# Kernel tuning notes

Measured on AMD Instinct MI355X. Metric: run time of the kernel, lower is better.

The kernel has to match this reference:

```python
import jax, jax.numpy as jnp
import numpy as np

MAX_ITER = 10
EPS = 1e-4


def setup_inputs() -> dict:
    key = jax.random.key(0)
    k1, k2, k3 = jax.random.split(key, 3)
    B, N, M = 64, 1024, 1024
    s = jax.random.uniform(k1, (B, N, M), dtype=jnp.float32)
    nrows = jax.random.randint(k2, (B,), 0, N, dtype=jnp.int64 if jax.config.read('jax_enable_x64') else jnp.int32)
    ncols = jax.random.randint(k3, (B,), 0, M, dtype=nrows.dtype)
    return {"s": s, "nrows": nrows, "ncols": ncols}


def _sinkhorn(s, nrows, ncols):
    # Faithful to torch Sinkhorn.forward with exp=False, dummy_row=False.
    # The torch code builds [B,N,N]/[B,M,M] block-of-ones matrices and matmuls;
    # mathematically this is a masked column-sum (even iters) / row-sum (odd iters)
    # over the valid nrows[b] x ncols[b] block, followed by division inside the
    # block and zeroing outside it.
    B, N, M = s.shape
    row_mask = jnp.arange(N)[None, :] < nrows[:, None]            # [B, N]
    col_mask = jnp.arange(M)[None, :] < ncols[:, None]            # [B, M]
    mask = row_mask[:, :, None] & col_mask[:, None, :]            # [B, N, M]

    out = s + EPS
    for i in range(MAX_ITER):
        if i % 2 == 0:
            # column sums over valid rows -> [B, 1, M]
            sm = jnp.sum(jnp.where(row_mask[:, :, None], out, 0.0), axis=1, keepdims=True)
        else:
            # row sums over valid cols -> [B, N, 1]
            sm = jnp.sum(jnp.where(col_mask[:, None, :], out, 0.0), axis=2, keepdims=True)
        sm = jnp.where(sm == 0, 1.0, sm)  # guard (only affects masked-out entries)
        out = jnp.where(mask, out / sm, 0.0)
    return out


def reference(s, nrows, ncols):
    return _sinkhorn(s, nrows, ncols)
```

## Files before the change

### kernel.cpp

```cpp
#include <hip/hip_runtime.h>
#include <hip/hip_fp16.h>

#define EPS 1e-4f
constexpr int N_DIM = 1024;
constexpr int M_DIM = 1024;
constexpr int BATCH = 64;
constexpr int CH    = 16;
constexpr int CROWS = N_DIM / CH;


__global__ __launch_bounds__(256)
void conv_col0(const float* __restrict__ s,
               const int* __restrict__ nrows,
               const int* __restrict__ ncols,
               __half* __restrict__ h,
               float* __restrict__ tp0) {
    const int b  = blockIdx.y;
    const int mt = blockIdx.x & 3;
    const int ch = blockIdx.x >> 2;
    const int R = nrows[b], C = ncols[b];
    const int n0 = ch * CROWS;
    if (n0 >= R) return;
    const int lane = threadIdx.x & 63, wv = threadIdx.x >> 6;
    const int m = mt * 256 + lane * 4;
    const int nend = min(R, n0 + CROWS);
    const size_t base = (size_t)b * N_DIM * M_DIM;

    float4 acc = make_float4(0.f, 0.f, 0.f, 0.f);
    if (mt * 256 < C) {
        for (int n = n0 + wv; n < nend; n += 4) {
            float4 v = *(const float4*)(s + base + (size_t)n * M_DIM + m);
            v.x = (m + 0 < C) ? v.x + EPS : 0.f;
            v.y = (m + 1 < C) ? v.y + EPS : 0.f;
            v.z = (m + 2 < C) ? v.z + EPS : 0.f;
            v.w = (m + 3 < C) ? v.w + EPS : 0.f;
            acc.x += v.x; acc.y += v.y; acc.z += v.z; acc.w += v.w;
            union { __half2 h2[2]; uint2 u2; } pk;
            pk.h2[0] = __floats2half2_rn(v.x, v.y);
            pk.h2[1] = __floats2half2_rn(v.z, v.w);
            *(uint2*)(h + base + (size_t)n * M_DIM + m) = pk.u2;
        }
    } else {
        const uint2 z = make_uint2(0u, 0u);
        for (int n = n0 + wv; n < nend; n += 4)
            *(uint2*)(h + base + (size_t)n * M_DIM + m) = z;
    }
    __shared__ float4 red[4][64];
    red[wv][lane] = acc;
    __syncthreads();
    if (wv == 0) {
        float4 a0 = red[0][lane], a1 = red[1][lane],
               a2 = red[2][lane], a3 = red[3][lane];
        float4 t = make_float4(a0.x + a1.x + a2.x + a3.x,
                               a0.y + a1.y + a2.y + a3.y,
                               a0.z + a1.z + a2.z + a3.z,
                               a0.w + a1.w + a2.w + a3.w);
        *(float4*)(tp0 + (size_t)(ch * BATCH + b) * M_DIM + m) = t;
    }
}

template <bool FINAL>
__global__ __launch_bounds__(256)
void row_step(const __half* __restrict__ h,
              const int* __restrict__ nrows,
              const int* __restrict__ ncols,
              const float* __restrict__ tpIn,
              float* __restrict__ tpOut,
              float* __restrict__ out) {
    const int b  = blockIdx.y;
    const int ch = blockIdx.x;
    const int R = nrows[b], C = ncols[b];
    const int n0 = ch * CROWS;
    if (!FINAL && n0 >= R) return;
    const int lane = threadIdx.x & 63, wv = threadIdx.x >> 6;
    const size_t base = (size_t)b * N_DIM * M_DIM;
    const bool hi = (C > 512);
    const bool anyrows = (n0 < R);

    __shared__ float clds[M_DIM];
    __shared__ float tp_lds[4][M_DIM];

    float crlo[8], crhi[8];
    if (anyrows) {
        const int nch = min(CH, (R + CROWS - 1) / CROWS);
        const int t4 = threadIdx.x * 4;
        if (hi || t4 < 512) {
            float4 sum = make_float4(0.f, 0.f, 0.f, 0.f);
            for (int cc = 0; cc < nch; ++cc) {
                float4 p = *(const float4*)(tpIn + (size_t)(cc * BATCH + b) * M_DIM + t4);
                sum.x += p.x; sum.y += p.y; sum.z += p.z; sum.w += p.w;
            }
            float4 cv;
            cv.x = (sum.x == 0.f) ? 1.f : 1.f / sum.x;
            cv.y = (sum.y == 0.f) ? 1.f : 1.f / sum.y;
            cv.z = (sum.z == 0.f) ? 1.f : 1.f / sum.z;
            cv.w = (sum.w == 0.f) ? 1.f : 1.f / sum.w;
            *(float4*)&clds[t4] = cv;
        }
        __syncthreads();
        {
            float4 a = *(const float4*)&clds[lane * 8];
            float4 bb = *(const float4*)&clds[lane * 8 + 4];
            crlo[0]=a.x; crlo[1]=a.y; crlo[2]=a.z; crlo[3]=a.w;
            crlo[4]=bb.x; crlo[5]=bb.y; crlo[6]=bb.z; crlo[7]=bb.w;
            if (hi) {
                float4 d = *(const float4*)&clds[512 + lane * 8];
                float4 e = *(const float4*)&clds[512 + lane * 8 + 4];
                crhi[0]=d.x; crhi[1]=d.y; crhi[2]=d.z; crhi[3]=d.w;
                crhi[4]=e.x; crhi[5]=e.y; crhi[6]=e.z; crhi[7]=e.w;
            }
        }
    }

    float tplo[8] = {0,0,0,0,0,0,0,0};
    float tphi[8] = {0,0,0,0,0,0,0,0};

    for (int i = 0; i < 16; ++i) {
        const int n = n0 + wv * 16 + i;
        if (n < R) {
            const __half* hrow = h + base + (size_t)n * M_DIM;
            uint4 rlo = *(const uint4*)(hrow + lane * 8);
            float flo[8];
            {
                const __half2* hp = (const __half2*)&rlo;
#pragma unroll
                for (int k = 0; k < 4; ++k) {
                    float2 f = __half22float2(hp[k]);
                    flo[2*k] = f.x; flo[2*k+1] = f.y;
                }
            }
            float dot = 0.f;
#pragma unroll
            for (int k = 0; k < 8; ++k) dot += flo[k] * crlo[k];
            float fhi[8];
            if (hi) {
                uint4 rhi = *(const uint4*)(hrow + 512 + lane * 8);
                const __half2* hq = (const __half2*)&rhi;
#pragma unroll
                for (int k = 0; k < 4; ++k) {
                    float2 f = __half22float2(hq[k]);
                    fhi[2*k] = f.x; fhi[2*k+1] = f.y;
                }
#pragma unroll
                for (int k = 0; k < 8; ++k) dot += fhi[k] * crhi[k];
            }
#pragma unroll
            for (int off = 32; off; off >>= 1) dot += __shfl_xor(dot, off);
            const float r = (dot == 0.f) ? 1.f : 1.f / dot;

            if (FINAL) {
                float* orow = out + base + (size_t)n * M_DIM;
                float4 o0 = make_float4(flo[0]*r*crlo[0], flo[1]*r*crlo[1],
                                        flo[2]*r*crlo[2], flo[3]*r*crlo[3]);
                float4 o1 = make_float4(flo[4]*r*crlo[4], flo[5]*r*crlo[5],
                                        flo[6]*r*crlo[6], flo[7]*r*crlo[7]);
                *(float4*)(orow + lane * 8)     = o0;
                *(float4*)(orow + lane * 8 + 4) = o1;
                float4 o2 = make_float4(0.f,0.f,0.f,0.f), o3 = o2;
                if (hi) {
                    o2 = make_float4(fhi[0]*r*crhi[0], fhi[1]*r*crhi[1],
                                     fhi[2]*r*crhi[2], fhi[3]*r*crhi[3]);
                    o3 = make_float4(fhi[4]*r*crhi[4], fhi[5]*r*crhi[5],
                                     fhi[6]*r*crhi[6], fhi[7]*r*crhi[7]);
                }
                *(float4*)(orow + 512 + lane * 8)     = o2;
                *(float4*)(orow + 512 + lane * 8 + 4) = o3;
            } else {
#pragma unroll
                for (int k = 0; k < 8; ++k) tplo[k] += flo[k] * r;
                if (hi) {
#pragma unroll
                    for (int k = 0; k < 8; ++k) tphi[k] += fhi[k] * r;
                }
            }
        } else if (FINAL) {
            float* orow = out + base + (size_t)n * M_DIM;
            const float4 z = make_float4(0.f, 0.f, 0.f, 0.f);
            *(float4*)(orow + lane * 8)           = z;
            *(float4*)(orow + lane * 8 + 4)       = z;
            *(float4*)(orow + 512 + lane * 8)     = z;
            *(float4*)(orow + 512 + lane * 8 + 4) = z;
        }
    }

    if (!FINAL) {
#pragma unroll
        for (int k = 0; k < 8; ++k) tp_lds[wv][lane * 8 + k] = tplo[k];
        if (hi) {
#pragma unroll
            for (int k = 0; k < 8; ++k) tp_lds[wv][512 + lane * 8 + k] = tphi[k];
        }
        __syncthreads();
        const int t4 = threadIdx.x * 4;
        if (hi || t4 < 512) {
            float4 s0 = *(const float4*)&tp_lds[0][t4];
            float4 s1 = *(const float4*)&tp_lds[1][t4];
            float4 s2 = *(const float4*)&tp_lds[2][t4];
            float4 s3 = *(const float4*)&tp_lds[3][t4];
            float4 t = make_float4(s0.x+s1.x+s2.x+s3.x, s0.y+s1.y+s2.y+s3.y,
                                   s0.z+s1.z+s2.z+s3.z, s0.w+s1.w+s2.w+s3.w);
            *(float4*)(tpOut + (size_t)(ch * BATCH + b) * M_DIM + t4) = t;
        }
    }
}

template <bool FIRST, int CHUNKS>
__global__ __launch_bounds__(256)
void col_sweep(const float* __restrict__ s, const int* __restrict__ nrows,
               const int* __restrict__ ncols, const float* __restrict__ u,
               float* __restrict__ tpart) {
    const int b  = blockIdx.y;
    const int mt = blockIdx.x & 3;
    const int ch = blockIdx.x >> 2;
    const int R = nrows[b], C = ncols[b];
    const int lane = threadIdx.x & 63, wv = threadIdx.x >> 6;
    const int m0 = mt * 256;
    const int m  = m0 + lane * 4;
    constexpr int RW = N_DIM / CHUNKS;
    const int n0 = ch * RW;
    const int nend = min(R, n0 + RW);

    __shared__ float rlds[RW > 1024 ? 1 : RW];
    if (!FIRST) {
        for (int i = threadIdx.x; i < RW; i += 256) {
            float uu = u[b * N_DIM + n0 + i];
            rlds[i] = (uu == 0.f) ? 1.f : 1.f / uu;
        }
        __syncthreads();
    }
    float4 acc = make_float4(0.f, 0.f, 0.f, 0.f);
    if (m0 < C) {
        const float* __restrict__ sb = s + (size_t)b * N_DIM * M_DIM;
#pragma unroll 4
        for (int n = n0 + wv; n < nend; n += 4) {
            float4 v = *(const float4*)(sb + (size_t)n * M_DIM + m);
            float rn = FIRST ? 1.f : rlds[n - n0];
            acc.x += rn * (v.x + EPS); acc.y += rn * (v.y + EPS);
            acc.z += rn * (v.z + EPS); acc.w += rn * (v.w + EPS);
        }
    }
    __shared__ float4 red[4][64];
    red[wv][lane] = acc;
    __syncthreads();
    if (wv == 0) {
        float4 a0 = red[0][lane], a1 = red[1][lane],
               a2 = red[2][lane], a3 = red[3][lane];
        float4 t = make_float4(a0.x + a1.x + a2.x + a3.x, a0.y + a1.y + a2.y + a3.y,
                               a0.z + a1.z + a2.z + a3.z, a0.w + a1.w + a2.w + a3.w);
        *(float4*)(tpart + ((size_t)(ch * BATCH + b)) * M_DIM + m) = t;
    }
}

template <int CHUNKS, bool WRITE_C>
__global__ __launch_bounds__(256)
void row_sweep(const float* __restrict__ s, const int* __restrict__ nrows,
               const int* __restrict__ ncols, const float* __restrict__ tpart,
               float* __restrict__ u, float* __restrict__ cOut) {
    const int b = blockIdx.y;
    const int R = nrows[b], C = ncols[b];
    const int n0 = blockIdx.x * 16;
    if (n0 >= R) return;
    __shared__ float clds[M_DIM];
    {
        const int t4 = threadIdx.x;
        float4 sum = make_float4(0.f, 0.f, 0.f, 0.f);
#pragma unroll
        for (int ch = 0; ch < CHUNKS; ++ch) {
            float4 p = *(const float4*)(tpart + ((size_t)(ch * BATCH + b)) * M_DIM + t4 * 4);
            sum.x += p.x; sum.y += p.y; sum.z += p.z; sum.w += p.w;
        }
        float4 cv;
        cv.x = (sum.x == 0.f) ? 1.f : 1.f / sum.x;
        cv.y = (sum.y == 0.f) ? 1.f : 1.f / sum.y;
        cv.z = (sum.z == 0.f) ? 1.f : 1.f / sum.z;
        cv.w = (sum.w == 0.f) ? 1.f : 1.f / sum.w;
        *(float4*)&clds[t4 * 4] = cv;
        if (WRITE_C && blockIdx.x == 0)
            *(float4*)(cOut + b * M_DIM + t4 * 4) = cv;
    }
    __syncthreads();
    const int lane = threadIdx.x & 63, wv = threadIdx.x >> 6;
    const int C4 = C >> 2;
#pragma unroll
    for (int i = 0; i < 4; ++i) {
        const int n = n0 + wv * 4 + i;
        if (n >= R) break;
        const float* __restrict__ srow = s + ((size_t)b * N_DIM + n) * M_DIM;
        float sum = 0.f;
        for (int j = lane; j < C4; j += 64) {
            float4 v  = ((const float4*)srow)[j];
            float4 cc = *(const float4*)&clds[j * 4];
            sum += (v.x + EPS) * cc.x + (v.y + EPS) * cc.y +
                   (v.z + EPS) * cc.z + (v.w + EPS) * cc.w;
        }
        for (int mm = (C4 << 2) + lane; mm < C; mm += 64)
            sum += (srow[mm] + EPS) * clds[mm];
#pragma unroll
        for (int off = 32; off; off >>= 1) sum += __shfl_down(sum, off);
        if (lane == 0) u[b * N_DIM + n] = sum;
    }
}

__global__ __launch_bounds__(256)
void finalize(const float* __restrict__ s, const int* __restrict__ nrows,
              const int* __restrict__ ncols, const float* __restrict__ u,
              const float* __restrict__ c, float* __restrict__ out) {
    const int n = blockIdx.x;
    const int b = blockIdx.y;
    const int R = nrows[b], C = ncols[b];
    const size_t base = ((size_t)b * N_DIM + n) * M_DIM;
    const int m = threadIdx.x * 4;

    float4 o = make_float4(0.f, 0.f, 0.f, 0.f);
    if (n < R && m < C) {
        float uu = u[b * N_DIM + n];
        float rn = (uu == 0.f) ? 1.f : 1.f / uu;
        float4 v  = *(const float4*)(s + base + m);
        float4 cc = *(const float4*)(c + b * M_DIM + m);
        o.x = (m + 0 < C) ? (v.x + EPS) * rn * cc.x : 0.f;
        o.y = (m + 1 < C) ? (v.y + EPS) * rn * cc.y : 0.f;
        o.z = (m + 2 < C) ? (v.z + EPS) * rn * cc.z : 0.f;
        o.w = (m + 3 < C) ? (v.w + EPS) * rn * cc.w : 0.f;
    }
    *(float4*)(out + base + m) = o;
}

extern "C" void kernel_launch(void* const* d_in, const int* in_sizes, int n_in,
                              void* d_out, int out_size, void* d_ws, size_t ws_size,
                              hipStream_t stream) {
    const float* s     = (const float*)d_in[0];
    const int*   nrows = (const int*)d_in[1];
    const int*   ncols = (const int*)d_in[2];
    float*       out   = (float*)d_out;

    const size_t hElems   = (size_t)BATCH * N_DIM * M_DIM;
    const size_t tpElems  = (size_t)CH * BATCH * M_DIM;
    const size_t need_f16 = hElems * 2 + 2 * tpElems * 4;

    if (ws_size >= need_f16) {
        __half* h   = (__half*)d_ws;
        float*  tp0 = (float*)(h + hElems);
        float*  tp1 = tp0 + tpElems;

        dim3 convGrid(4 * CH, BATCH);
        dim3 kGrid(CH, BATCH);

        conv_col0<<<convGrid, 256, 0, stream>>>(s, nrows, ncols, h, tp0);
        row_step<false><<<kGrid, 256, 0, stream>>>(h, nrows, ncols, tp0, tp1, out);
        row_step<false><<<kGrid, 256, 0, stream>>>(h, nrows, ncols, tp1, tp0, out);
        row_step<false><<<kGrid, 256, 0, stream>>>(h, nrows, ncols, tp0, tp1, out);
        row_step<false><<<kGrid, 256, 0, stream>>>(h, nrows, ncols, tp1, tp0, out);
        row_step<true ><<<kGrid, 256, 0, stream>>>(h, nrows, ncols, tp0, tp1, out);
        return;
    }

    const size_t need4 = (size_t)(4 * BATCH * M_DIM + BATCH * N_DIM + BATCH * M_DIM) * 4;
    float* tpart = (float*)d_ws;
    if (ws_size >= need4) {
        float* u = tpart + (size_t)4 * BATCH * M_DIM;
        float* c = u + (size_t)BATCH * N_DIM;
        dim3 colGrid(16, BATCH), rowGrid(64, BATCH);
        col_sweep<true, 4><<<colGrid, 256, 0, stream>>>(s, nrows, ncols, u, tpart);
        row_sweep<4, false><<<rowGrid, 256, 0, stream>>>(s, nrows, ncols, tpart, u, c);
        for (int k = 1; k < 4; ++k) {
            col_sweep<false, 4><<<colGrid, 256, 0, stream>>>(s, nrows, ncols, u, tpart);
            row_sweep<4, false><<<rowGrid, 256, 0, stream>>>(s, nrows, ncols, tpart, u, c);
        }
        col_sweep<false, 4><<<colGrid, 256, 0, stream>>>(s, nrows, ncols, u, tpart);
        row_sweep<4, true><<<rowGrid, 256, 0, stream>>>(s, nrows, ncols, tpart, u, c);
        finalize<<<dim3(N_DIM, BATCH), 256, 0, stream>>>(s, nrows, ncols, u, c, out);
    } else {
        float* u = tpart + (size_t)BATCH * M_DIM;
        float* c = u + (size_t)BATCH * N_DIM;
        dim3 colGrid(4, BATCH), rowGrid(64, BATCH);
        col_sweep<true, 1><<<colGrid, 256, 0, stream>>>(s, nrows, ncols, u, tpart);
        row_sweep<1, false><<<rowGrid, 256, 0, stream>>>(s, nrows, ncols, tpart, u, c);
        for (int k = 1; k < 4; ++k) {
            col_sweep<false, 1><<<colGrid, 256, 0, stream>>>(s, nrows, ncols, u, tpart);
            row_sweep<1, false><<<rowGrid, 256, 0, stream>>>(s, nrows, ncols, tpart, u, c);
        }
        col_sweep<false, 1><<<colGrid, 256, 0, stream>>>(s, nrows, ncols, u, tpart);
        row_sweep<1, true><<<rowGrid, 256, 0, stream>>>(s, nrows, ncols, tpart, u, c);
        finalize<<<dim3(N_DIM, BATCH), 256, 0, stream>>>(s, nrows, ncols, u, c, out);
    }
}
```

Measured before the change: 210.4 us.

## Fuse all Sinkhorn phases into one cooperative kernel with per-batch barriers

Replaces the six-launch pipeline (conversion plus five row steps) with a single cooperative kernel. Blocks of the same batch synchronise through global atomic counters between phases. This removes kernel launch gaps and keeps each block's fp16 rows hot in cache between iterations. It adds spin-wait barrier costs and requires every block to be co-resident, checked through an occupancy query, with the old multi-kernel path kept as fallback. The fp32 fallback paths for small workspaces are removed.

```diff
diff --git a/kernel.cpp b/kernel.cpp
--- a/kernel.cpp
+++ b/kernel.cpp
@@ -2,18 +2,278 @@
 #include <hip/hip_fp16.h>
 
 #define EPS 1e-4f
-constexpr int N_DIM = 1024;
-constexpr int M_DIM = 1024;
-constexpr int BATCH = 64;
-constexpr int CH    = 16;
-constexpr int CROWS = N_DIM / CH;
-
+constexpr int N_DIM  = 1024;
+constexpr int M_DIM  = 1024;
+constexpr int BATCH  = 64;
+constexpr int CH     = 16;
+constexpr int CROWS  = N_DIM / CH;
+constexpr int NPHASE = 5;
+
+
+__global__ void zero_cnt(unsigned int* cnt) {
+    const int t = threadIdx.x;
+    if (t < NPHASE * BATCH) cnt[t] = 0u;
+}
+
+__device__ __forceinline__ void bat_barrier(unsigned int* cnt, int idx,
+                                            unsigned int nact) {
+    __syncthreads();
+    if (threadIdx.x == 0) {
+        __threadfence();
+        atomicAdd(&cnt[idx], 1u);
+        while (__hip_atomic_load(&cnt[idx], __ATOMIC_ACQUIRE,
+                                 __HIP_MEMORY_SCOPE_AGENT) < nact)
+            __builtin_amdgcn_s_sleep(8);
+    }
+    __syncthreads();
+    __threadfence();
+}
+
+__global__ __launch_bounds__(256, 4)
+void sinkhorn_one(const float* __restrict__ s,
+                  const int* __restrict__ nrows,
+                  const int* __restrict__ ncols,
+                  __half* __restrict__ h,
+                  float* __restrict__ tp0,
+                  float* __restrict__ tp1,
+                  unsigned int* __restrict__ cnt,
+                  float* __restrict__ out)
+{
+    const int b  = blockIdx.y;
+    const int ch = blockIdx.x;
+    const int R = nrows[b], C = ncols[b];
+    const int n0 = ch * CROWS;
+    const size_t base = (size_t)b * N_DIM * M_DIM;
+    const int tid = threadIdx.x, lane = tid & 63, wv = tid >> 6;
+
+    if (n0 >= R) {
+        const float4 z = make_float4(0.f, 0.f, 0.f, 0.f);
+        for (int i = 0; i < CROWS; ++i)
+            *(float4*)(out + base + (size_t)(n0 + i) * M_DIM + tid * 4) = z;
+        return;
+    }
+
+    const unsigned int nact = (unsigned int)((R + CROWS - 1) / CROWS);
+    const int nend = min(R, n0 + CROWS);
+    const bool hi = (C > 512);
+
+    __shared__ float clds[M_DIM];
+    __shared__ float tp_lds[4][M_DIM];
+
+    {
+        const int m = tid * 4;
+        float4 acc = make_float4(0.f, 0.f, 0.f, 0.f);
+        if (m < C) {
+            for (int n = n0; n < nend; ++n) {
+                float4 v = *(const float4*)(s + base + (size_t)n * M_DIM + m);
+                v.x += EPS;
+                v.y = (m + 1 < C) ? v.y + EPS : 0.f;
+                v.z = (m + 2 < C) ? v.z + EPS : 0.f;
+                v.w = (m + 3 < C) ? v.w + EPS : 0.f;
+                acc.x += v.x; acc.y += v.y; acc.z += v.z; acc.w += v.w;
+                union { __half2 h2[2]; uint2 u2; } pk;
+                pk.h2[0] = __floats2half2_rn(v.x, v.y);
+                pk.h2[1] = __floats2half2_rn(v.z, v.w);
+                *(uint2*)(h + base + (size_t)n * M_DIM + m) = pk.u2;
+            }
+        } else if (m < 512 || hi) {
+            const uint2 z = make_uint2(0u, 0u);
+            for (int n = n0; n < nend; ++n)
+                *(uint2*)(h + base + (size_t)n * M_DIM + m) = z;
+        }
+        *(float4*)(tp0 + (size_t)(ch * BATCH + b) * M_DIM + m) = acc;
+    }
+    bat_barrier(cnt, 0 * BATCH + b, nact);
+
+    const float* tpIn = tp0;
+    float*       tpOut = tp1;
+
+    float crlo[8], crhi[8];
+
+    for (int step = 0; step < 4; ++step) {
+        {
+            const int m = tid * 4;
+            if (m < 512 || hi) {
+                float4 sum = make_float4(0.f, 0.f, 0.f, 0.f);
+                for (unsigned int cc = 0; cc < nact; ++cc) {
+                    float4 p = *(const float4*)(tpIn + (size_t)(cc * BATCH + b) * M_DIM + m);
+                    sum.x += p.x; sum.y += p.y; sum.z += p.z; sum.w += p.w;
+                }
+                float4 cv;
+                cv.x = (sum.x == 0.f) ? 1.f : 1.f / sum.x;
+                cv.y = (sum.y == 0.f) ? 1.f : 1.f / sum.y;
+                cv.z = (sum.z == 0.f) ? 1.f : 1.f / sum.z;
+                cv.w = (sum.w == 0.f) ? 1.f : 1.f / sum.w;
+                *(float4*)&clds[m] = cv;
+            }
+        }
+        __syncthreads();
+        {
+            float4 a  = *(const float4*)&clds[lane * 8];
+            float4 bb = *(const float4*)&clds[lane * 8 + 4];
+            crlo[0]=a.x; crlo[1]=a.y; crlo[2]=a.z; crlo[3]=a.w;
+            crlo[4]=bb.x; crlo[5]=bb.y; crlo[6]=bb.z; crlo[7]=bb.w;
+            if (hi) {
+                float4 d = *(const float4*)&clds[512 + lane * 8];
+                float4 e = *(const float4*)&clds[512 + lane * 8 + 4];
+                crhi[0]=d.x; crhi[1]=d.y; crhi[2]=d.z; crhi[3]=d.w;
+                crhi[4]=e.x; crhi[5]=e.y; crhi[6]=e.z; crhi[7]=e.w;
+            }
+        }
+
+        float tplo[8] = {0,0,0,0,0,0,0,0};
+        float tphi[8] = {0,0,0,0,0,0,0,0};
+
+        for (int i = 0; i < 16; ++i) {
+            const int n = n0 + wv * 16 + i;
+            if (n >= R) break;
+            const __half* hrow = h + base + (size_t)n * M_DIM;
+            uint4 rlo = *(const uint4*)(hrow + lane * 8);
+            float flo[8], fhi[8];
+            {
+                const __half2* hp = (const __half2*)&rlo;
+#pragma unroll
+                for (int k = 0; k < 4; ++k) {
+                    float2 f = __half22float2(hp[k]);
+                    flo[2*k] = f.x; flo[2*k+1] = f.y;
+                }
+            }
+            float dot = 0.f;
+#pragma unroll
+            for (int k = 0; k < 8; ++k) dot += flo[k] * crlo[k];
+            if (hi) {
+                uint4 rhi = *(const uint4*)(hrow + 512 + lane * 8);
+                const __half2* hq = (const __half2*)&rhi;
+#pragma unroll
+                for (int k = 0; k < 4; ++k) {
+                    float2 f = __half22float2(hq[k]);
+                    fhi[2*k] = f.x; fhi[2*k+1] = f.y;
+                }
+#pragma unroll
+                for (int k = 0; k < 8; ++k) dot += fhi[k] * crhi[k];
+            }
+#pragma unroll
+            for (int off = 32; off; off >>= 1) dot += __shfl_xor(dot, off);
+            const float r = (dot == 0.f) ? 1.f : 1.f / dot;
+#pragma unroll
+            for (int k = 0; k < 8; ++k) tplo[k] += flo[k] * r;
+            if (hi) {
+#pragma unroll
+                for (int k = 0; k < 8; ++k) tphi[k] += fhi[k] * r;
+            }
+        }
+
+#pragma unroll
+        for (int k = 0; k < 8; ++k) tp_lds[wv][lane * 8 + k] = tplo[k];
+        if (hi) {
+#pragma unroll
+            for (int k = 0; k < 8; ++k) tp_lds[wv][512 + lane * 8 + k] = tphi[k];
+        }
+        __syncthreads();
+        {
+            const int m = tid * 4;
+            if (m < 512 || hi) {
+                float4 s0 = *(const float4*)&tp_lds[0][m];
+                float4 s1 = *(const float4*)&tp_lds[1][m];
+                float4 s2 = *(const float4*)&tp_lds[2][m];
+                float4 s3 = *(const float4*)&tp_lds[3][m];
+                float4 t = make_float4(s0.x+s1.x+s2.x+s3.x, s0.y+s1.y+s2.y+s3.y,
+                                       s0.z+s1.z+s2.z+s3.z, s0.w+s1.w+s2.w+s3.w);
+                *(float4*)(tpOut + (size_t)(ch * BATCH + b) * M_DIM + m) = t;
+            }
+        }
+        bat_barrier(cnt, (1 + step) * BATCH + b, nact);
+        const float* ti = tpOut; tpOut = (float*)tpIn; tpIn = ti;
+    }
+
+    {
+        const int m = tid * 4;
+        if (m < 512 || hi) {
+            float4 sum = make_float4(0.f, 0.f, 0.f, 0.f);
+            for (unsigned int cc = 0; cc < nact; ++cc) {
+                float4 p = *(const float4*)(tpIn + (size_t)(cc * BATCH + b) * M_DIM + m);
+                sum.x += p.x; sum.y += p.y; sum.z += p.z; sum.w += p.w;
+            }
+            float4 cv;
+            cv.x = (sum.x == 0.f) ? 1.f : 1.f / sum.x;
+            cv.y = (sum.y == 0.f) ? 1.f : 1.f / sum.y;
+            cv.z = (sum.z == 0.f) ? 1.f : 1.f / sum.z;
+            cv.w = (sum.w == 0.f) ? 1.f : 1.f / sum.w;
+            *(float4*)&clds[m] = cv;
+        }
+    }
+    __syncthreads();
+    {
+        float4 a  = *(const float4*)&clds[lane * 8];
+        float4 bb = *(const float4*)&clds[lane * 8 + 4];
+        crlo[0]=a.x; crlo[1]=a.y; crlo[2]=a.z; crlo[3]=a.w;
+        crlo[4]=bb.x; crlo[5]=bb.y; crlo[6]=bb.z; crlo[7]=bb.w;
+        if (hi) {
+            float4 d = *(const float4*)&clds[512 + lane * 8];
+            float4 e = *(const float4*)&clds[512 + lane * 8 + 4];
+            crhi[0]=d.x; crhi[1]=d.y; crhi[2]=d.z; crhi[3]=d.w;
+            crhi[4]=e.x; crhi[5]=e.y; crhi[6]=e.z; crhi[7]=e.w;
+        }
+    }
+    const float4 z4 = make_float4(0.f, 0.f, 0.f, 0.f);
+    for (int i = 0; i < 16; ++i) {
+        const int n = n0 + wv * 16 + i;
+        float* orow = out + base + (size_t)n * M_DIM;
+        if (n < R) {
+            const __half* hrow = h + base + (size_t)n * M_DIM;
+            uint4 rlo = *(const uint4*)(hrow + lane * 8);
+            float flo[8], fhi[8];
+            {
+                const __half2* hp = (const __half2*)&rlo;
+#pragma unroll
+                for (int k = 0; k < 4; ++k) {
+                    float2 f = __half22float2(hp[k]);
+                    flo[2*k] = f.x; flo[2*k+1] = f.y;
+                }
+            }
+            float dot = 0.f;
+#pragma unroll
+            for (int k = 0; k < 8; ++k) dot += flo[k] * crlo[k];
+            if (hi) {
+                uint4 rhi = *(const uint4*)(hrow + 512 + lane * 8);
+                const __half2* hq = (const __half2*)&rhi;
+#pragma unroll
+                for (int k = 0; k < 4; ++k) {
+                    float2 f = __half22float2(hq[k]);
+                    fhi[2*k] = f.x; fhi[2*k+1] = f.y;
+                }
+#pragma unroll
+                for (int k = 0; k < 8; ++k) dot += fhi[k] * crhi[k];
+            }
+#pragma unroll
+            for (int off = 32; off; off >>= 1) dot += __shfl_xor(dot, off);
+            const float r = (dot == 0.f) ? 1.f : 1.f / dot;
+
+            *(float4*)(orow + lane * 8)     = make_float4(flo[0]*r*crlo[0], flo[1]*r*crlo[1],
+                                                          flo[2]*r*crlo[2], flo[3]*r*crlo[3]);
+            *(float4*)(orow + lane * 8 + 4) = make_float4(flo[4]*r*crlo[4], flo[5]*r*crlo[5],
+                                                          flo[6]*r*crlo[6], flo[7]*r*crlo[7]);
+            float4 o2 = z4, o3 = z4;
+            if (hi) {
+                o2 = make_float4(fhi[0]*r*crhi[0], fhi[1]*r*crhi[1],
+                                 fhi[2]*r*crhi[2], fhi[3]*r*crhi[3]);
+                o3 = make_float4(fhi[4]*r*crhi[4], fhi[5]*r*crhi[5],
+                                 fhi[6]*r*crhi[6], fhi[7]*r*crhi[7]);
+            }
+            *(float4*)(orow + 512 + lane * 8)     = o2;
+            *(float4*)(orow + 512 + lane * 8 + 4) = o3;
+        } else {
+            *(float4*)(orow + lane * 8)           = z4;
+            *(float4*)(orow + lane * 8 + 4)       = z4;
+            *(float4*)(orow + 512 + lane * 8)     = z4;
+            *(float4*)(orow + 512 + lane * 8 + 4) = z4;
+        }
+    }
+}
 
 __global__ __launch_bounds__(256)
-void conv_col0(const float* __restrict__ s,
-               const int* __restrict__ nrows,
-               const int* __restrict__ ncols,
-               __half* __restrict__ h,
+void conv_col0(const float* __restrict__ s, const int* __restrict__ nrows,
+               const int* __restrict__ ncols, __half* __restrict__ h,
                float* __restrict__ tp0) {
     const int b  = blockIdx.y;
     const int mt = blockIdx.x & 3;
@@ -51,22 +311,17 @@
     if (wv == 0) {
         float4 a0 = red[0][lane], a1 = red[1][lane],
                a2 = red[2][lane], a3 = red[3][lane];
-        float4 t = make_float4(a0.x + a1.x + a2.x + a3.x,
-                               a0.y + a1.y + a2.y + a3.y,
-                               a0.z + a1.z + a2.z + a3.z,
-                               a0.w + a1.w + a2.w + a3.w);
-        *(float4*)(tp0 + (size_t)(ch * BATCH + b) * M_DIM + m) = t;
+        *(float4*)(tp0 + (size_t)(ch * BATCH + b) * M_DIM + m) =
+            make_float4(a0.x+a1.x+a2.x+a3.x, a0.y+a1.y+a2.y+a3.y,
+                        a0.z+a1.z+a2.z+a3.z, a0.w+a1.w+a2.w+a3.w);
     }
 }
 
 template <bool FINAL>
 __global__ __launch_bounds__(256)
-void row_step(const __half* __restrict__ h,
-              const int* __restrict__ nrows,
-              const int* __restrict__ ncols,
-              const float* __restrict__ tpIn,
-              float* __restrict__ tpOut,
-              float* __restrict__ out) {
+void row_step(const __half* __restrict__ h, const int* __restrict__ nrows,
+              const int* __restrict__ ncols, const float* __restrict__ tpIn,
+              float* __restrict__ tpOut, float* __restrict__ out) {
     const int b  = blockIdx.y;
     const int ch = blockIdx.x;
     const int R = nrows[b], C = ncols[b];
@@ -98,17 +353,15 @@
             *(float4*)&clds[t4] = cv;
         }
         __syncthreads();
-        {
-            float4 a = *(const float4*)&clds[lane * 8];
-            float4 bb = *(const float4*)&clds[lane * 8 + 4];
-            crlo[0]=a.x; crlo[1]=a.y; crlo[2]=a.z; crlo[3]=a.w;
-            crlo[4]=bb.x; crlo[5]=bb.y; crlo[6]=bb.z; crlo[7]=bb.w;
-            if (hi) {
-                float4 d = *(const float4*)&clds[512 + lane * 8];
-                float4 e = *(const float4*)&clds[512 + lane * 8 + 4];
-                crhi[0]=d.x; crhi[1]=d.y; crhi[2]=d.z; crhi[3]=d.w;
-                crhi[4]=e.x; crhi[5]=e.y; crhi[6]=e.z; crhi[7]=e.w;
-            }
+        float4 a = *(const float4*)&clds[lane * 8];
+        float4 bb = *(const float4*)&clds[lane * 8 + 4];
+        crlo[0]=a.x; crlo[1]=a.y; crlo[2]=a.z; crlo[3]=a.w;
+        crlo[4]=bb.x; crlo[5]=bb.y; crlo[6]=bb.z; crlo[7]=bb.w;
+        if (hi) {
+            float4 d = *(const float4*)&clds[512 + lane * 8];
+            float4 e = *(const float4*)&clds[512 + lane * 8 + 4];
+            crhi[0]=d.x; crhi[1]=d.y; crhi[2]=d.z; crhi[3]=d.w;
+            crhi[4]=e.x; crhi[5]=e.y; crhi[6]=e.z; crhi[7]=e.w;
         }
     }
 
@@ -120,19 +373,16 @@
         if (n < R) {
             const __half* hrow = h + base + (size_t)n * M_DIM;
             uint4 rlo = *(const uint4*)(hrow + lane * 8);
-            float flo[8];
-            {
-                const __half2* hp = (const __half2*)&rlo;
-#pragma unroll
-                for (int k = 0; k < 4; ++k) {
-                    float2 f = __half22float2(hp[k]);
-                    flo[2*k] = f.x; flo[2*k+1] = f.y;
-                }
+            float flo[8], fhi[8];
+            const __half2* hp = (const __half2*)&rlo;
+#pragma unroll
+            for (int k = 0; k < 4; ++k) {
+                float2 f = __half22float2(hp[k]);
+                flo[2*k] = f.x; flo[2*k+1] = f.y;
             }
             float dot = 0.f;
 #pragma unroll
             for (int k = 0; k < 8; ++k) dot += flo[k] * crlo[k];
-            float fhi[8];
             if (hi) {
                 uint4 rhi = *(const uint4*)(hrow + 512 + lane * 8);
                 const __half2* hq = (const __half2*)&rhi;
@@ -150,12 +400,10 @@
 
             if (FINAL) {
                 float* orow = out + base + (size_t)n * M_DIM;
-                float4 o0 = make_float4(flo[0]*r*crlo[0], flo[1]*r*crlo[1],
-                                        flo[2]*r*crlo[2], flo[3]*r*crlo[3]);
-                float4 o1 = make_float4(flo[4]*r*crlo[4], flo[5]*r*crlo[5],
-                                        flo[6]*r*crlo[6], flo[7]*r*crlo[7]);
-                *(float4*)(orow + lane * 8)     = o0;
-                *(float4*)(orow + lane * 8 + 4) = o1;
+                *(float4*)(orow + lane * 8)     = make_float4(flo[0]*r*crlo[0], flo[1]*r*crlo[1],
+                                                              flo[2]*r*crlo[2], flo[3]*r*crlo[3]);
+                *(float4*)(orow + lane * 8 + 4) = make_float4(flo[4]*r*crlo[4], flo[5]*r*crlo[5],
+                                                              flo[6]*r*crlo[6], flo[7]*r*crlo[7]);
                 float4 o2 = make_float4(0.f,0.f,0.f,0.f), o3 = o2;
                 if (hi) {
                     o2 = make_float4(fhi[0]*r*crhi[0], fhi[1]*r*crhi[1],
@@ -197,132 +445,11 @@
             float4 s1 = *(const float4*)&tp_lds[1][t4];
             float4 s2 = *(const float4*)&tp_lds[2][t4];
             float4 s3 = *(const float4*)&tp_lds[3][t4];
-            float4 t = make_float4(s0.x+s1.x+s2.x+s3.x, s0.y+s1.y+s2.y+s3.y,
-                                   s0.z+s1.z+s2.z+s3.z, s0.w+s1.w+s2.w+s3.w);
-            *(float4*)(tpOut + (size_t)(ch * BATCH + b) * M_DIM + t4) = t;
-        }
-    }
-}
-
-template <bool FIRST, int CHUNKS>
-__global__ __launch_bounds__(256)
-void col_sweep(const float* __restrict__ s, const int* __restrict__ nrows,
-               const int* __restrict__ ncols, const float* __restrict__ u,
-               float* __restrict__ tpart) {
-    const int b  = blockIdx.y;
-    const int mt = blockIdx.x & 3;
-    const int ch = blockIdx.x >> 2;
-    const int R = nrows[b], C = ncols[b];
-    const int lane = threadIdx.x & 63, wv = threadIdx.x >> 6;
-    const int m0 = mt * 256;
-    const int m  = m0 + lane * 4;
-    constexpr int RW = N_DIM / CHUNKS;
-    const int n0 = ch * RW;
-    const int nend = min(R, n0 + RW);
-
-    __shared__ float rlds[RW > 1024 ? 1 : RW];
-    if (!FIRST) {
-        for (int i = threadIdx.x; i < RW; i += 256) {
-            float uu = u[b * N_DIM + n0 + i];
-            rlds[i] = (uu == 0.f) ? 1.f : 1.f / uu;
-        }
-        __syncthreads();
-    }
-    float4 acc = make_float4(0.f, 0.f, 0.f, 0.f);
-    if (m0 < C) {
-        const float* __restrict__ sb = s + (size_t)b * N_DIM * M_DIM;
-#pragma unroll 4
-        for (int n = n0 + wv; n < nend; n += 4) {
-            float4 v = *(const float4*)(sb + (size_t)n * M_DIM + m);
-            float rn = FIRST ? 1.f : rlds[n - n0];
-            acc.x += rn * (v.x + EPS); acc.y += rn * (v.y + EPS);
-            acc.z += rn * (v.z + EPS); acc.w += rn * (v.w + EPS);
-        }
-    }
-    __shared__ float4 red[4][64];
-    red[wv][lane] = acc;
-    __syncthreads();
-    if (wv == 0) {
-        float4 a0 = red[0][lane], a1 = red[1][lane],
-               a2 = red[2][lane], a3 = red[3][lane];
-        float4 t = make_float4(a0.x + a1.x + a2.x + a3.x, a0.y + a1.y + a2.y + a3.y,
-                               a0.z + a1.z + a2.z + a3.z, a0.w + a1.w + a2.w + a3.w);
-        *(float4*)(tpart + ((size_t)(ch * BATCH + b)) * M_DIM + m) = t;
-    }
-}
-
-template <int CHUNKS, bool WRITE_C>
-__global__ __launch_bounds__(256)
-void row_sweep(const float* __restrict__ s, const int* __restrict__ nrows,
-               const int* __restrict__ ncols, const float* __restrict__ tpart,
-               float* __restrict__ u, float* __restrict__ cOut) {
-    const int b = blockIdx.y;
-    const int R = nrows[b], C = ncols[b];
-    const int n0 = blockIdx.x * 16;
-    if (n0 >= R) return;
-    __shared__ float clds[M_DIM];
-    {
-        const int t4 = threadIdx.x;
-        float4 sum = make_float4(0.f, 0.f, 0.f, 0.f);
-#pragma unroll
-        for (int ch = 0; ch < CHUNKS; ++ch) {
-            float4 p = *(const float4*)(tpart + ((size_t)(ch * BATCH + b)) * M_DIM + t4 * 4);
-            sum.x += p.x; sum.y += p.y; sum.z += p.z; sum.w += p.w;
-        }
-        float4 cv;
-        cv.x = (sum.x == 0.f) ? 1.f : 1.f / sum.x;
-        cv.y = (sum.y == 0.f) ? 1.f : 1.f / sum.y;
-        cv.z = (sum.z == 0.f) ? 1.f : 1.f / sum.z;
-        cv.w = (sum.w == 0.f) ? 1.f : 1.f / sum.w;
-        *(float4*)&clds[t4 * 4] = cv;
-        if (WRITE_C && blockIdx.x == 0)
-            *(float4*)(cOut + b * M_DIM + t4 * 4) = cv;
-    }
-    __syncthreads();
-    const int lane = threadIdx.x & 63, wv = threadIdx.x >> 6;
-    const int C4 = C >> 2;
-#pragma unroll
-    for (int i = 0; i < 4; ++i) {
-        const int n = n0 + wv * 4 + i;
-        if (n >= R) break;
-        const float* __restrict__ srow = s + ((size_t)b * N_DIM + n) * M_DIM;
-        float sum = 0.f;
-        for (int j = lane; j < C4; j += 64) {
-            float4 v  = ((const float4*)srow)[j];
-            float4 cc = *(const float4*)&clds[j * 4];
-            sum += (v.x + EPS) * cc.x + (v.y + EPS) * cc.y +
-                   (v.z + EPS) * cc.z + (v.w + EPS) * cc.w;
-        }
-        for (int mm = (C4 << 2) + lane; mm < C; mm += 64)
-            sum += (srow[mm] + EPS) * clds[mm];
-#pragma unroll
-        for (int off = 32; off; off >>= 1) sum += __shfl_down(sum, off);
-        if (lane == 0) u[b * N_DIM + n] = sum;
-    }
-}
-
-__global__ __launch_bounds__(256)
-void finalize(const float* __restrict__ s, const int* __restrict__ nrows,
-              const int* __restrict__ ncols, const float* __restrict__ u,
-              const float* __restrict__ c, float* __restrict__ out) {
-    const int n = blockIdx.x;
-    const int b = blockIdx.y;
-    const int R = nrows[b], C = ncols[b];
-    const size_t base = ((size_t)b * N_DIM + n) * M_DIM;
-    const int m = threadIdx.x * 4;
-
-    float4 o = make_float4(0.f, 0.f, 0.f, 0.f);
-    if (n < R && m < C) {
-        float uu = u[b * N_DIM + n];
-        float rn = (uu == 0.f) ? 1.f : 1.f / uu;
-        float4 v  = *(const float4*)(s + base + m);
-        float4 cc = *(const float4*)(c + b * M_DIM + m);
-        o.x = (m + 0 < C) ? (v.x + EPS) * rn * cc.x : 0.f;
-        o.y = (m + 1 < C) ? (v.y + EPS) * rn * cc.y : 0.f;
-        o.z = (m + 2 < C) ? (v.z + EPS) * rn * cc.z : 0.f;
-        o.w = (m + 3 < C) ? (v.w + EPS) * rn * cc.w : 0.f;
-    }
-    *(float4*)(out + base + m) = o;
+            *(float4*)(tpOut + (size_t)(ch * BATCH + b) * M_DIM + t4) =
+                make_float4(s0.x+s1.x+s2.x+s3.x, s0.y+s1.y+s2.y+s3.y,
+                            s0.z+s1.z+s2.z+s3.z, s0.w+s1.w+s2.w+s3.w);
+        }
+    }
 }
 
 extern "C" void kernel_launch(void* const* d_in, const int* in_sizes, int n_in,
@@ -333,18 +460,31 @@
     const int*   ncols = (const int*)d_in[2];
     float*       out   = (float*)d_out;
 
-    const size_t hElems   = (size_t)BATCH * N_DIM * M_DIM;
-    const size_t tpElems  = (size_t)CH * BATCH * M_DIM;
-    const size_t need_f16 = hElems * 2 + 2 * tpElems * 4;
-
-    if (ws_size >= need_f16) {
+    const size_t hElems  = (size_t)BATCH * N_DIM * M_DIM;
+    const size_t tpElems = (size_t)CH * BATCH * M_DIM;
+    const size_t need    = hElems * 2 + 2 * tpElems * 4 + NPHASE * BATCH * 4;
+
+    if (ws_size >= need) {
         __half* h   = (__half*)d_ws;
         float*  tp0 = (float*)(h + hElems);
         float*  tp1 = tp0 + tpElems;
-
-        dim3 convGrid(4 * CH, BATCH);
-        dim3 kGrid(CH, BATCH);
-
+        unsigned int* cnt = (unsigned int*)(tp1 + tpElems);
+
+        int dev = 0, numCU = 0, perCU = 0;
+        hipGetDevice(&dev);
+        hipDeviceGetAttribute(&numCU, hipDeviceAttributeMultiprocessorCount, dev);
+        hipOccupancyMaxActiveBlocksPerMultiprocessor(&perCU, sinkhorn_one, 256, 0);
+
+        if ((long long)perCU * numCU >= CH * BATCH) {
+            zero_cnt<<<1, 320, 0, stream>>>(cnt);
+            void* args[] = {(void*)&s, (void*)&nrows, (void*)&ncols, (void*)&h,
+                            (void*)&tp0, (void*)&tp1, (void*)&cnt, (void*)&out};
+            hipLaunchCooperativeKernel((void*)sinkhorn_one, dim3(CH, BATCH),
+                                       dim3(256), args, 0, stream);
+            return;
+        }
+
+        dim3 convGrid(4 * CH, BATCH), kGrid(CH, BATCH);
         conv_col0<<<convGrid, 256, 0, stream>>>(s, nrows, ncols, h, tp0);
         row_step<false><<<kGrid, 256, 0, stream>>>(h, nrows, ncols, tp0, tp1, out);
         row_step<false><<<kGrid, 256, 0, stream>>>(h, nrows, ncols, tp1, tp0, out);
@@ -353,34 +493,4 @@
         row_step<true ><<<kGrid, 256, 0, stream>>>(h, nrows, ncols, tp0, tp1, out);
         return;
     }
-
-    const size_t need4 = (size_t)(4 * BATCH * M_DIM + BATCH * N_DIM + BATCH * M_DIM) * 4;
-    float* tpart = (float*)d_ws;
-    if (ws_size >= need4) {
-        float* u = tpart + (size_t)4 * BATCH * M_DIM;
-        float* c = u + (size_t)BATCH * N_DIM;
-        dim3 colGrid(16, BATCH), rowGrid(64, BATCH);
-        col_sweep<true, 4><<<colGrid, 256, 0, stream>>>(s, nrows, ncols, u, tpart);
-        row_sweep<4, false><<<rowGrid, 256, 0, stream>>>(s, nrows, ncols, tpart, u, c);
-        for (int k = 1; k < 4; ++k) {
-            col_sweep<false, 4><<<colGrid, 256, 0, stream>>>(s, nrows, ncols, u, tpart);
-            row_sweep<4, false><<<rowGrid, 256, 0, stream>>>(s, nrows, ncols, tpart, u, c);
-        }
-        col_sweep<false, 4><<<colGrid, 256, 0, stream>>>(s, nrows, ncols, u, tpart);
-        row_sweep<4, true><<<rowGrid, 256, 0, stream>>>(s, nrows, ncols, tpart, u, c);
-        finalize<<<dim3(N_DIM, BATCH), 256, 0, stream>>>(s, nrows, ncols, u, c, out);
-    } else {
-        float* u = tpart + (size_t)BATCH * M_DIM;
-        float* c = u + (size_t)BATCH * N_DIM;
-        dim3 colGrid(4, BATCH), rowGrid(64, BATCH);
-        col_sweep<true, 1><<<colGrid, 256, 0, stream>>>(s, nrows, ncols, u, tpart);
-        row_sweep<1, false><<<rowGrid, 256, 0, stream>>>(s, nrows, ncols, tpart, u, c);
-        for (int k = 1; k < 4; ++k) {
-            col_sweep<false, 1><<<colGrid, 256, 0, stream>>>(s, nrows, ncols, u, tpart);
-            row_sweep<1, false><<<rowGrid, 256, 0, stream>>>(s, nrows, ncols, tpart, u, c);
-        }
-        col_sweep<false, 1><<<colGrid, 256, 0, stream>>>(s, nrows, ncols, u, tpart);
-        row_sweep<1, true><<<rowGrid, 256, 0, stream>>>(s, nrows, ncols, tpart, u, c);
-        finalize<<<dim3(N_DIM, BATCH), 256, 0, stream>>>(s, nrows, ncols, u, c, out);
-    }
-}
+}
```

Result: no change. 207.3 us (-1.5%).
